# Kernel tuning notes

Hardware: AMD Instinct MI355X
Metric: run time of the kernel (lower is better)

The kernel has to match this reference:

```python
import jax, jax.numpy as jnp
import numpy as np

B, L, D = 2, 2048, 1024
H, QK, V = 8, 128, 128
EPS = 1e-5  # torch GroupNorm default


def setup_inputs() -> dict:
    key = jax.random.key(0)
    ks = jax.random.split(key, 6)
    sequence = jax.random.normal(ks[0], (B, L, D), jnp.float32)
    times = jnp.broadcast_to(jnp.arange(L, dtype=jnp.float32), (B, L))
    shift = D ** -0.5
    scale = 2.0 * shift
    w_q = jax.random.uniform(ks[1], (H, D, QK), jnp.float32) * scale - shift
    w_k = jax.random.uniform(ks[2], (H, D, QK), jnp.float32) * scale - shift
    w_v = jax.random.uniform(ks[3], (H, D, V), jnp.float32) * scale - shift
    out_dims = H * V
    w_g = jax.random.uniform(ks[4], (D, out_dims), jnp.float32) * scale - shift
    shift2 = out_dims ** -0.5
    scale2 = 2.0 * shift2
    w_o = jax.random.uniform(ks[5], (out_dims, out_dims), jnp.float32) * scale2 - shift2
    gn_w = jnp.ones((out_dims,), jnp.float32)
    gn_b = jnp.zeros((out_dims,), jnp.float32)
    return dict(sequence=sequence, times=times, w_q=w_q, w_k=w_k, w_v=w_v,
                w_g=w_g, w_o=w_o, gn_w=gn_w, gn_b=gn_b)


def rotate_by_i(x):
    # pairs (even, odd) -> (-odd, even), interleaved back
    x2 = x.reshape(x.shape[:-1] + (-1, 2))
    real, imag = x2[..., 0], x2[..., 1]
    return jnp.stack([-imag, real], axis=-1).reshape(x.shape)


def reference(sequence, times, w_q, w_k, w_v, w_g, w_o, gn_w, gn_b):
    gammas = 1.0 - 2.0 ** (-5.0 - jnp.arange(H, dtype=jnp.float32))            # (H,)
    thetas = 10000.0 ** (-2.0 * jnp.arange(QK // 2, dtype=jnp.float32) / QK)   # (QK/2,)

    q = jnp.einsum('bld,hdk->hblk', sequence, w_q)  # (H,B,L,QK)
    k = jnp.einsum('bld,hdk->hblk', sequence, w_k)
    v = jnp.einsum('bld,hdv->hblv', sequence, w_v)  # (H,B,L,V)

    # xPos rotor: angles interleaved-duplicated along last dim
    angles = times[..., None] * thetas              # (B,L,QK/2)
    cos = jnp.repeat(jnp.cos(angles), 2, axis=-1)   # (B,L,QK)
    sin = jnp.repeat(jnp.sin(angles), 2, axis=-1)
    q = cos * q + sin * rotate_by_i(q)
    k = cos * k - sin * rotate_by_i(k)

    # causal exponential-decay mask D[n,m] = gamma**(n-m) * (n>=m)
    mat = times[:, :, None] - times[:, None, :]     # (B,L,L)
    mask = mat >= 0
    g4 = gammas[:, None, None, None]                # (H,1,1,1)
    d = jnp.where(mask, g4 ** jnp.where(mask, mat, 0.0), 0.0)  # (H,B,L,L)

    ret = jnp.einsum('hbik,hbjk->hbij', q, k) * d   # (H,B,L,L)
    retention = jnp.einsum('hbij,hbjv->hbiv', ret, v)  # (H,B,L,V)

    # GroupNorm(num_heads, H*V): normalize each head's V channels per token
    r = jnp.transpose(retention, (1, 2, 0, 3))      # (B,L,H,V)
    mean = r.mean(-1, keepdims=True)
    var = r.var(-1, keepdims=True)
    rn = (r - mean) / jnp.sqrt(var + EPS)
    rn = rn * gn_w.reshape(H, V) + gn_b.reshape(H, V)
    rn = rn.reshape(B, L, H * V)

    g = sequence @ w_g
    gate = g * jax.nn.sigmoid(g)                    # swish
    return (gate * rn) @ w_o                        # (B,L,H*V)
```

## Files before the change

### kernel.cpp

```cpp
#include <hip/hip_runtime.h>
#include <stdint.h>

typedef unsigned short u16;
typedef unsigned int   u32;
typedef short  short8 __attribute__((ext_vector_type(8)));
typedef float  f32x4  __attribute__((ext_vector_type(4)));

#define DEV static __device__ __forceinline__

DEV float bf2f(u16 u) { u32 x = ((u32)u) << 16; float f; __builtin_memcpy(&f, &x, 4); return f; }
DEV u16 f2bf(float f) {
  u32 u; __builtin_memcpy(&u, &f, 4);
  return (u16)((u + 0x7FFFu + ((u >> 16) & 1u)) >> 16);
}
DEV bool probe_bf16(const void* times) { return *(const u32*)times == 0x3F800000u; }

DEV void gload16(const u16* g, u16* l) {
  __builtin_amdgcn_global_load_lds(
      (__attribute__((address_space(1))) void*)(u16*)g,
      (__attribute__((address_space(3))) void*)l, 16, 0, 0);
}

DEV f32x4 MFMA(short8 a, short8 b, f32x4 c) {
  return __builtin_amdgcn_mfma_f32_16x16x32_bf16(a, b, c, 0, 0, 0);
}

DEV void gemm128(const u16* Ag, const u16* Bg, int K, u16* sA, u16* sB,
                 f32x4 (&acc)[4][4]) {
  const int tid = threadIdx.x;
  const int lane = tid & 63, w = tid >> 6;
  const int wm = w >> 1, wn = w & 1;
  const int row = lane & 15, quad = lane >> 4;
  f32x4 z = {0.f, 0.f, 0.f, 0.f};
#pragma unroll
  for (int mt = 0; mt < 4; ++mt)
#pragma unroll
    for (int nt = 0; nt < 4; ++nt) acc[mt][nt] = z;

  for (int k0 = 0; k0 < K; k0 += 64) {
    __syncthreads();
#pragma unroll
    for (int i = 0; i < 4; ++i) {
      int c = (w << 2) + i;
      gload16(Ag + (size_t)(c * 8 + (lane >> 3)) * K + k0 + (lane & 7) * 8, sA + c * 544);
      gload16(Bg + (size_t)(c * 8 + (lane >> 3)) * K + k0 + (lane & 7) * 8, sB + c * 544);
    }
    __syncthreads();
#pragma unroll
    for (int kt = 0; kt < 2; ++kt) {
      short8 av[4], bv[4];
#pragma unroll
      for (int t = 0; t < 4; ++t) {
        int m = wm * 64 + t * 16 + row;
        av[t] = *(const short8*)(sA + (m >> 3) * 544 + (m & 7) * 64 + kt * 32 + quad * 8);
        int n = wn * 64 + t * 16 + row;
        bv[t] = *(const short8*)(sB + (n >> 3) * 544 + (n & 7) * 64 + kt * 32 + quad * 8);
      }
#pragma unroll
      for (int mt = 0; mt < 4; ++mt)
#pragma unroll
        for (int nt = 0; nt < 4; ++nt)
          acc[mt][nt] = MFMA(av[mt], bv[nt], acc[mt][nt]);
    }
  }
}

__global__ __launch_bounds__(256) void transpose_kernel(
    const void* wq, const void* wk, const void* wv, const void* wg,
    const void* wo, const void* times, u16* wsT) {
  __shared__ u16 T[128 * 132];
  int s = blockIdx.x, t = blockIdx.y;
  bool isbf = probe_bf16(times);
  const void* src; int ld; size_t off0;
  if (s < 8)       { src = wq; ld = 128;  off0 = (size_t)s * 131072; }
  else if (s < 16) { src = wk; ld = 128;  off0 = (size_t)(s - 8) * 131072; }
  else if (s < 24) { src = wv; ld = 128;  off0 = (size_t)(s - 16) * 131072; }
  else if (s < 32) { src = wg; ld = 1024; off0 = (size_t)(s - 24) * 128; }
  else             { src = wo; ld = 1024; off0 = (size_t)(s - 32) * 128; }
  int d0 = t * 128;
  const u16* s16 = (const u16*)src;
  const float* s32 = (const float*)src;
  for (int pass = 0; pass < 64; ++pass) {
    int idx = pass * 256 + threadIdx.x;
    int dl = idx >> 7, c = idx & 127;
    size_t goff = off0 + (size_t)(d0 + dl) * ld + c;
    T[c * 132 + dl] = isbf ? s16[goff] : f2bf(s32[goff]);
  }
  __syncthreads();
  u16* dst = wsT + (size_t)s * 131072;
  for (int pass = 0; pass < 16; ++pass) {
    int idx = pass * 256 + threadIdx.x;
    int c = idx >> 5, ch = idx & 31;
    uint2 v = *(const uint2*)&T[c * 132 + ch * 4];
    *(uint2*)&dst[(size_t)c * 1024 + d0 + ch * 4] = v;
  }
}

__global__ __launch_bounds__(256) void seq_kernel(const void* seq, const void* times, u16* dst) {
  bool isbf = probe_bf16(times);
  size_t idx = ((size_t)blockIdx.x * 256 + threadIdx.x) * 8;
  if (isbf) {
    *(uint4*)&dst[idx] = *(const uint4*)((const u16*)seq + idx);
  } else {
    const float* s = (const float*)seq;
    u32 a0 = (u32)f2bf(s[idx + 0]) | ((u32)f2bf(s[idx + 1]) << 16);
    u32 a1 = (u32)f2bf(s[idx + 2]) | ((u32)f2bf(s[idx + 3]) << 16);
    u32 a2 = (u32)f2bf(s[idx + 4]) | ((u32)f2bf(s[idx + 5]) << 16);
    u32 a3 = (u32)f2bf(s[idx + 6]) | ((u32)f2bf(s[idx + 7]) << 16);
    uint4 v; v.x = a0; v.y = a1; v.z = a2; v.w = a3;
    *(uint4*)&dst[idx] = v;
  }
}

__global__ __launch_bounds__(256, 2) void proj_kernel(
    const u16* seqb, const void* times, const u16* wsT,
    u16* qws, u16* kws, u16* vtws, u16* gatews) {
  __shared__ __align__(16) u16 smem[17408];
  u16* sA = smem;
  u16* sB = smem + 8704;
  int nb = blockIdx.x, mb = blockIdx.y;
  f32x4 acc[4][4];
  gemm128(seqb + (size_t)mb * 128 * 1024, wsT + (size_t)nb * 131072, 1024, sA, sB, acc);

  const int tid = threadIdx.x, lane = tid & 63, w = tid >> 6;
  const int wm = w >> 1, wn = w & 1, row = lane & 15, quad = lane >> 4;
  const bool isbf = probe_bf16(times);
  const u16* t16 = (const u16*)times;
  const float* t32 = (const float*)times;
  const int b = mb >> 4, l0 = (mb & 15) * 128;

  __syncthreads();

  if (nb < 16) {
    int type = nb >> 3;
    int h = nb & 7;
    float sgnk = type ? -1.f : 1.f;
#pragma unroll
    for (int mt = 0; mt < 4; ++mt) {
#pragma unroll
      for (int nt = 0; nt < 4; ++nt) {
        int c = wn * 64 + nt * 16 + row;
        float theta = exp2f(-0.2076205059304601f * (float)(c >> 1));
        float sgn = (c & 1) ? 1.f : -1.f;
#pragma unroll
        for (int r = 0; r < 4; ++r) {
          int lloc = wm * 64 + mt * 16 + quad * 4 + r;
          float v = acc[mt][nt][r];
          float pv = __shfl_xor(v, 1);
          float tv = isbf ? bf2f(t16[b * 2048 + l0 + lloc]) : t32[b * 2048 + l0 + lloc];
          float rev = theta * tv * 0.15915494309189535f;
          rev -= floorf(rev);
          float sn = __builtin_amdgcn_sinf(rev);
          float cs = __builtin_amdgcn_cosf(rev);
          float ov = cs * v + sgnk * sgn * sn * pv;
          u16 o16 = f2bf(ov);
          int other = __shfl_xor((int)o16, 1);
          if (!(lane & 1))
            *(u32*)&smem[lloc * 136 + c] = (u32)o16 | ((u32)other << 16);
        }
      }
    }
    __syncthreads();
    u16* outp = (type ? kws : qws) + (((size_t)(h * 2 + b) * 2048 + l0) << 7);
#pragma unroll
    for (int p = 0; p < 8; ++p) {
      int idx = p * 256 + tid, rr = idx >> 4, ch = idx & 15;
      *(uint4*)&outp[(size_t)rr * 128 + ch * 8] = *(const uint4*)&smem[rr * 136 + ch * 8];
    }
  } else if (nb < 24) {
    int h = nb & 7;
#pragma unroll
    for (int mt = 0; mt < 4; ++mt) {
      int lb = wm * 64 + mt * 16 + quad * 4;
#pragma unroll
      for (int nt = 0; nt < 4; ++nt) {
        int c = wn * 64 + nt * 16 + row;
        uint2 pk;
        pk.x = (u32)f2bf(acc[mt][nt][0]) | ((u32)f2bf(acc[mt][nt][1]) << 16);
        pk.y = (u32)f2bf(acc[mt][nt][2]) | ((u32)f2bf(acc[mt][nt][3]) << 16);
        *(uint2*)&smem[c * 136 + lb] = pk;
      }
    }
    __syncthreads();
    u16* outp = vtws + (size_t)(h * 2 + b) * 262144 + l0;
#pragma unroll
    for (int p = 0; p < 8; ++p) {
      int idx = p * 256 + tid, cc = idx >> 4, ch = idx & 15;
      *(uint4*)&outp[(size_t)cc * 2048 + ch * 8] = *(const uint4*)&smem[cc * 136 + ch * 8];
    }
  } else {
    int cb = nb - 24;
#pragma unroll
    for (int mt = 0; mt < 4; ++mt) {
#pragma unroll
      for (int nt = 0; nt < 4; ++nt) {
        int c = wn * 64 + nt * 16 + row;
#pragma unroll
        for (int r = 0; r < 4; ++r) {
          int lloc = wm * 64 + mt * 16 + quad * 4 + r;
          float x = acc[mt][nt][r];
          float s = x / (1.f + __expf(-x));
          u16 o16 = f2bf(s);
          int other = __shfl_xor((int)o16, 1);
          if (!(lane & 1))
            *(u32*)&smem[lloc * 136 + c] = (u32)o16 | ((u32)other << 16);
        }
      }
    }
    __syncthreads();
    u16* outp = gatews + (size_t)(mb * 128) * 1024 + (size_t)cb * 128;
#pragma unroll
    for (int p = 0; p < 8; ++p) {
      int idx = p * 256 + tid, rr = idx >> 4, ch = idx & 15;
      *(uint4*)&outp[(size_t)rr * 1024 + ch * 8] = *(const uint4*)&smem[rr * 136 + ch * 8];
    }
  }
}

__global__ __launch_bounds__(256, 2) void retention_kernel(
    const u16* qws, const u16* kws, const u16* vtws, const void* times, float* rws) {
  __shared__ __align__(16) u16 smem[17408 + 16896];
  u16* sKP = smem;
  u16* sV  = smem + 17408;

  const int ib = (int)blockIdx.x >> 1;
  const int par = (int)blockIdx.x & 1;

  const int hb = blockIdx.y;
  const int h = hb >> 1, b = hb & 1;
  const int i0 = ib * 128;
  const int tid = threadIdx.x, lane = tid & 63, w = tid >> 6;
  const int wm = w >> 1, wn = w & 1, row = lane & 15, quad = lane >> 4;
  const bool isbf = probe_bf16(times);
  const u16* t16 = (const u16*)times;
  const float* t32 = (const float*)times;
  const float gamma = 1.f - exp2f(-5.f - (float)h);
  const float l2g = log2f(gamma);

  short8 qf[4][4];
  const u16* qbase = qws + ((size_t)hb * 2048 + i0) * 128;
#pragma unroll
  for (int mt = 0; mt < 4; ++mt)
#pragma unroll
    for (int kt = 0; kt < 4; ++kt)
      qf[mt][kt] = *(const short8*)(qbase + (size_t)(wm * 64 + mt * 16 + row) * 128 + kt * 32 + quad * 8);

  float rpow[4][4];
#pragma unroll
  for (int mt = 0; mt < 4; ++mt)
#pragma unroll
    for (int r = 0; r < 4; ++r) {
      int i = i0 + wm * 64 + mt * 16 + quad * 4 + r;
      float tv = isbf ? bf2f(t16[b * 2048 + i]) : t32[b * 2048 + i];
      rpow[mt][r] = exp2f(l2g * (tv - (float)i0));
    }

  f32x4 z = {0.f, 0.f, 0.f, 0.f};
  f32x4 oacc[4][4];
#pragma unroll
  for (int mt = 0; mt < 4; ++mt)
#pragma unroll
    for (int nt = 0; nt < 4; ++nt) oacc[mt][nt] = z;

  const u16* kbase = kws + (size_t)hb * 262144;
  const u16* vbase = vtws + (size_t)hb * 262144;

  for (int jb = par; jb <= ib; jb += 2) {
    const int j0 = jb * 128;
    if (l2g * (float)(i0 - j0 - 258) < -57.f) continue;
    __syncthreads();
#pragma unroll
    for (int ii = 0; ii < 8; ++ii) {
      int c = w * 8 + ii;
      gload16(kbase + (size_t)(j0 + c * 4 + (lane >> 4)) * 128 + (lane & 15) * 8, sKP + c * 528);
      gload16(vbase + (size_t)(c * 4 + (lane >> 4)) * 2048 + j0 + (lane & 15) * 8, sV + c * 528);
    }
    __syncthreads();

    f32x4 p[4][4];
#pragma unroll
    for (int mt = 0; mt < 4; ++mt)
#pragma unroll
      for (int nt = 0; nt < 4; ++nt) p[mt][nt] = z;
#pragma unroll
    for (int kt = 0; kt < 4; ++kt) {
      short8 bv[4];
#pragma unroll
      for (int nt = 0; nt < 4; ++nt) {
        int jr = wn * 64 + nt * 16 + row;
        bv[nt] = *(const short8*)(sKP + (jr >> 2) * 528 + (jr & 3) * 128 + kt * 32 + quad * 8);
      }
#pragma unroll
      for (int mt = 0; mt < 4; ++mt)
#pragma unroll
        for (int nt = 0; nt < 4; ++nt)
          p[mt][nt] = MFMA(qf[mt][kt], bv[nt], p[mt][nt]);
    }
    __syncthreads();

    float cp[4];
#pragma unroll
    for (int nt = 0; nt < 4; ++nt) {
      int j = j0 + wn * 64 + nt * 16 + row;
      float tv = isbf ? bf2f(t16[b * 2048 + j]) : t32[b * 2048 + j];
      cp[nt] = exp2f(l2g * ((float)i0 - tv));
    }
    bool intra = (jb == ib);
#pragma unroll
    for (int mt = 0; mt < 4; ++mt)
#pragma unroll
      for (int nt = 0; nt < 4; ++nt)
#pragma unroll
        for (int r = 0; r < 4; ++r) {
          float f = rpow[mt][r] * cp[nt];
          float val = p[mt][nt][r] * f;
          if (intra && (f > 1.00001f)) val = 0.f;
          sKP[(wm * 64 + mt * 16 + quad * 4 + r) * 136 + wn * 64 + nt * 16 + row] = f2bf(val);
        }
    __syncthreads();

#pragma unroll
    for (int kt = 0; kt < 4; ++kt) {
      short8 av[4], bv[4];
#pragma unroll
      for (int mt = 0; mt < 4; ++mt)
        av[mt] = *(const short8*)(sKP + (wm * 64 + mt * 16 + row) * 136 + kt * 32 + quad * 8);
#pragma unroll
      for (int nt = 0; nt < 4; ++nt) {
        int v = wn * 64 + nt * 16 + row;
        bv[nt] = *(const short8*)(sV + (v >> 2) * 528 + (v & 3) * 128 + kt * 32 + quad * 8);
      }
#pragma unroll
      for (int mt = 0; mt < 4; ++mt)
#pragma unroll
        for (int nt = 0; nt < 4; ++nt)
          oacc[mt][nt] = MFMA(av[mt], bv[nt], oacc[mt][nt]);
    }
  }

  float* rp = rws + (size_t)par * 4194304 + ((size_t)hb * 2048 + i0) * 128;
#pragma unroll
  for (int mt = 0; mt < 4; ++mt)
#pragma unroll
    for (int nt = 0; nt < 4; ++nt)
#pragma unroll
      for (int r = 0; r < 4; ++r) {
        int i = wm * 64 + mt * 16 + quad * 4 + r;
        int v = wn * 64 + nt * 16 + row;
        rp[(size_t)i * 128 + v] = oacc[mt][nt][r];
      }
}

__global__ __launch_bounds__(256) void norm_kernel(
    const float* rws, const u16* gatews, const void* gnw, const void* gnb,
    const void* times, u16* xws) {
  int tid = threadIdx.x, lane = tid & 63, w = tid >> 6;
  int rid = blockIdx.x * 4 + w;
  int hb = rid >> 11, l = rid & 2047, h = hb >> 1, b = hb & 1;
  bool isbf = probe_bf16(times);
  float2 a0 = *(const float2*)&rws[(size_t)rid * 128 + lane * 2];
  float2 a1 = *(const float2*)&rws[(size_t)4194304 + (size_t)rid * 128 + lane * 2];
  float x0 = a0.x + a1.x, x1 = a0.y + a1.y;
  float s = x0 + x1, ss = x0 * x0 + x1 * x1;
#pragma unroll
  for (int o = 1; o < 64; o <<= 1) { s += __shfl_xor(s, o); ss += __shfl_xor(ss, o); }
  float mean = s * (1.f / 128.f);
  float var = fmaxf(ss * (1.f / 128.f) - mean * mean, 0.f);
  float inv = rsqrtf(var + 1e-5f);
  int c0 = h * 128 + lane * 2;
  float g0, g1, bb0, bb1;
  if (isbf) {
    g0 = bf2f(((const u16*)gnw)[c0]); g1 = bf2f(((const u16*)gnw)[c0 + 1]);
    bb0 = bf2f(((const u16*)gnb)[c0]); bb1 = bf2f(((const u16*)gnb)[c0 + 1]);
  } else {
    g0 = ((const float*)gnw)[c0]; g1 = ((const float*)gnw)[c0 + 1];
    bb0 = ((const float*)gnb)[c0]; bb1 = ((const float*)gnb)[c0 + 1];
  }
  float y0 = (x0 - mean) * inv * g0 + bb0;
  float y1 = (x1 - mean) * inv * g1 + bb1;
  size_t xi = ((size_t)(b * 2048 + l)) * 1024 + c0;
  float gt0 = bf2f(gatews[xi]), gt1 = bf2f(gatews[xi + 1]);
  u32 pk = (u32)f2bf(y0 * gt0) | ((u32)f2bf(y1 * gt1) << 16);
  *(u32*)&xws[xi] = pk;
}

__global__ __launch_bounds__(256, 2) void out_kernel(
    const u16* xws, const u16* wsT, const void* times, void* dout) {
  __shared__ __align__(16) u16 smem[17408];
  u16* sA = smem;
  u16* sB = smem + 8704;
  int nb = blockIdx.x, mb = blockIdx.y;
  f32x4 acc[4][4];
  gemm128(xws + (size_t)mb * 128 * 1024, wsT + (size_t)(32 + nb) * 131072, 1024, sA, sB, acc);
  const int tid = threadIdx.x, lane = tid & 63, w = tid >> 6;
  const int wm = w >> 1, wn = w & 1, row = lane & 15, quad = lane >> 4;
  bool isbf = probe_bf16(times);
  if (isbf) {
    __syncthreads();
#pragma unroll
    for (int mt = 0; mt < 4; ++mt) {
#pragma unroll
      for (int nt = 0; nt < 4; ++nt) {
        int c = wn * 64 + nt * 16 + row;
#pragma unroll
        for (int r = 0; r < 4; ++r) {
          int lloc = wm * 64 + mt * 16 + quad * 4 + r;
          u16 o16 = f2bf(acc[mt][nt][r]);
          int other = __shfl_xor((int)o16, 1);
          if (!(lane & 1))
            *(u32*)&smem[lloc * 136 + c] = (u32)o16 | ((u32)other << 16);
        }
      }
    }
    __syncthreads();
    u16* outp = (u16*)dout + (size_t)(mb * 128) * 1024 + (size_t)nb * 128;
#pragma unroll
    for (int p = 0; p < 8; ++p) {
      int idx = p * 256 + tid, rr = idx >> 4, ch = idx & 15;
      *(uint4*)&outp[(size_t)rr * 1024 + ch * 8] = *(const uint4*)&smem[rr * 136 + ch * 8];
    }
  } else {
#pragma unroll
    for (int mt = 0; mt < 4; ++mt)
#pragma unroll
      for (int nt = 0; nt < 4; ++nt)
#pragma unroll
        for (int r = 0; r < 4; ++r) {
          int i = mb * 128 + wm * 64 + mt * 16 + quad * 4 + r;
          size_t o = (size_t)i * 1024 + nb * 128 + wn * 64 + nt * 16 + row;
          ((float*)dout)[o] = acc[mt][nt][r];
        }
  }
}

extern "C" void kernel_launch(void* const* d_in, const int* in_sizes, int n_in,
                              void* d_out, int out_size, void* d_ws, size_t ws_size,
                              hipStream_t stream) {
  const void* seq   = d_in[0];
  const void* times = d_in[1];
  const void* wq = d_in[2];
  const void* wk = d_in[3];
  const void* wv = d_in[4];
  const void* wg = d_in[5];
  const void* wo = d_in[6];
  const void* gnw = d_in[7];
  const void* gnb = d_in[8];

  u16* ws = (u16*)d_ws;
  u16* wsT    = ws;
  u16* qws    = ws + 5242880;
  u16* kws    = qws + 4194304;
  u16* vtws   = kws + 4194304;
  u16* gatews = vtws + 4194304;
  float* rws  = (float*)(gatews + 4194304);
  u16* seqb   = (u16*)(rws + 8388608);
  u16* xws    = qws;

  transpose_kernel<<<dim3(40, 8), 256, 0, stream>>>(wq, wk, wv, wg, wo, times, wsT);
  seq_kernel<<<dim3(2048), 256, 0, stream>>>(seq, times, seqb);
  proj_kernel<<<dim3(32, 32), 256, 0, stream>>>(seqb, times, wsT, qws, kws, vtws, gatews);
  retention_kernel<<<dim3(32, 16), 256, 0, stream>>>(qws, kws, vtws, times, rws);
  norm_kernel<<<dim3(8192), 256, 0, stream>>>(rws, gatews, gnw, gnb, times, xws);
  out_kernel<<<dim3(8, 32), 256, 0, stream>>>(xws, wsT, times, d_out);
}
```

Baseline: 274.1 us.

## Halve retention query tile to 64 rows and schedule heavy blocks first

The retention kernel now gives each block 64 query rows instead of 128, doubling the grid. Each warp owns 16 rows across all 128 key or value columns, replacing the 2x2 warp split. Block indices are reversed so blocks with the most key tiles launch first, which should improve load balance and CU fill across the causal triangle. The cost is that each K/V tile staged in LDS is reused over half as many query rows, so K/V global traffic and B-fragment LDS reads per MFMA increase.

```diff
diff --git a/kernel.cpp b/kernel.cpp
--- a/kernel.cpp
+++ b/kernel.cpp
@@ -219,53 +219,49 @@
 
 __global__ __launch_bounds__(256, 2) void retention_kernel(
     const u16* qws, const u16* kws, const u16* vtws, const void* times, float* rws) {
-  __shared__ __align__(16) u16 smem[17408 + 16896];
+  __shared__ __align__(16) u16 smem[16896 * 2];
   u16* sKP = smem;
-  u16* sV  = smem + 17408;
-
-  const int ib = (int)blockIdx.x >> 1;
-  const int par = (int)blockIdx.x & 1;
+  u16* sV  = smem + 16896;
+
+  const int x = 63 - (int)blockIdx.x;
+  const int ib = x >> 1;
+  const int par = x & 1;
+  const int jb_max = ib >> 1;
 
   const int hb = blockIdx.y;
   const int h = hb >> 1, b = hb & 1;
-  const int i0 = ib * 128;
+  const int i0 = ib * 64;
   const int tid = threadIdx.x, lane = tid & 63, w = tid >> 6;
-  const int wm = w >> 1, wn = w & 1, row = lane & 15, quad = lane >> 4;
+  const int row = lane & 15, quad = lane >> 4;
   const bool isbf = probe_bf16(times);
   const u16* t16 = (const u16*)times;
   const float* t32 = (const float*)times;
   const float gamma = 1.f - exp2f(-5.f - (float)h);
   const float l2g = log2f(gamma);
 
-  short8 qf[4][4];
-  const u16* qbase = qws + ((size_t)hb * 2048 + i0) * 128;
-#pragma unroll
-  for (int mt = 0; mt < 4; ++mt)
-#pragma unroll
-    for (int kt = 0; kt < 4; ++kt)
-      qf[mt][kt] = *(const short8*)(qbase + (size_t)(wm * 64 + mt * 16 + row) * 128 + kt * 32 + quad * 8);
-
-  float rpow[4][4];
-#pragma unroll
-  for (int mt = 0; mt < 4; ++mt)
-#pragma unroll
-    for (int r = 0; r < 4; ++r) {
-      int i = i0 + wm * 64 + mt * 16 + quad * 4 + r;
-      float tv = isbf ? bf2f(t16[b * 2048 + i]) : t32[b * 2048 + i];
-      rpow[mt][r] = exp2f(l2g * (tv - (float)i0));
-    }
+  short8 qf[4];
+  const u16* qrow = qws + ((size_t)hb * 2048 + i0 + w * 16 + row) * 128;
+#pragma unroll
+  for (int kt = 0; kt < 4; ++kt)
+    qf[kt] = *(const short8*)(qrow + kt * 32 + quad * 8);
+
+  float rpow[4];
+#pragma unroll
+  for (int r = 0; r < 4; ++r) {
+    int i = i0 + w * 16 + quad * 4 + r;
+    float tv = isbf ? bf2f(t16[b * 2048 + i]) : t32[b * 2048 + i];
+    rpow[r] = exp2f(l2g * (tv - (float)i0));
+  }
 
   f32x4 z = {0.f, 0.f, 0.f, 0.f};
-  f32x4 oacc[4][4];
-#pragma unroll
-  for (int mt = 0; mt < 4; ++mt)
-#pragma unroll
-    for (int nt = 0; nt < 4; ++nt) oacc[mt][nt] = z;
+  f32x4 oacc[8];
+#pragma unroll
+  for (int nt = 0; nt < 8; ++nt) oacc[nt] = z;
 
   const u16* kbase = kws + (size_t)hb * 262144;
   const u16* vbase = vtws + (size_t)hb * 262144;
 
-  for (int jb = par; jb <= ib; jb += 2) {
+  for (int jb = par; jb <= jb_max; jb += 2) {
     const int j0 = jb * 128;
     if (l2g * (float)(i0 - j0 - 258) < -57.f) continue;
     __syncthreads();
@@ -277,78 +273,66 @@
     }
     __syncthreads();
 
-    f32x4 p[4][4];
-#pragma unroll
-    for (int mt = 0; mt < 4; ++mt)
-#pragma unroll
-      for (int nt = 0; nt < 4; ++nt) p[mt][nt] = z;
+    f32x4 p[8];
+#pragma unroll
+    for (int nt = 0; nt < 8; ++nt) p[nt] = z;
 #pragma unroll
     for (int kt = 0; kt < 4; ++kt) {
-      short8 bv[4];
-#pragma unroll
-      for (int nt = 0; nt < 4; ++nt) {
-        int jr = wn * 64 + nt * 16 + row;
+      short8 bv[8];
+#pragma unroll
+      for (int nt = 0; nt < 8; ++nt) {
+        int jr = nt * 16 + row;
         bv[nt] = *(const short8*)(sKP + (jr >> 2) * 528 + (jr & 3) * 128 + kt * 32 + quad * 8);
       }
 #pragma unroll
-      for (int mt = 0; mt < 4; ++mt)
-#pragma unroll
-        for (int nt = 0; nt < 4; ++nt)
-          p[mt][nt] = MFMA(qf[mt][kt], bv[nt], p[mt][nt]);
-    }
-    __syncthreads();
-
-    float cp[4];
-#pragma unroll
-    for (int nt = 0; nt < 4; ++nt) {
-      int j = j0 + wn * 64 + nt * 16 + row;
+      for (int nt = 0; nt < 8; ++nt)
+        p[nt] = MFMA(qf[kt], bv[nt], p[nt]);
+    }
+    __syncthreads();
+
+    float cp[8];
+#pragma unroll
+    for (int nt = 0; nt < 8; ++nt) {
+      int j = j0 + nt * 16 + row;
       float tv = isbf ? bf2f(t16[b * 2048 + j]) : t32[b * 2048 + j];
       cp[nt] = exp2f(l2g * ((float)i0 - tv));
     }
-    bool intra = (jb == ib);
-#pragma unroll
-    for (int mt = 0; mt < 4; ++mt)
-#pragma unroll
-      for (int nt = 0; nt < 4; ++nt)
-#pragma unroll
-        for (int r = 0; r < 4; ++r) {
-          float f = rpow[mt][r] * cp[nt];
-          float val = p[mt][nt][r] * f;
-          if (intra && (f > 1.00001f)) val = 0.f;
-          sKP[(wm * 64 + mt * 16 + quad * 4 + r) * 136 + wn * 64 + nt * 16 + row] = f2bf(val);
-        }
+    bool intra = (jb == jb_max);
+#pragma unroll
+    for (int nt = 0; nt < 8; ++nt)
+#pragma unroll
+      for (int r = 0; r < 4; ++r) {
+        float f = rpow[r] * cp[nt];
+        float val = p[nt][r] * f;
+        if (intra && (f > 1.00001f)) val = 0.f;
+        sKP[(w * 16 + quad * 4 + r) * 136 + nt * 16 + row] = f2bf(val);
+      }
     __syncthreads();
 
 #pragma unroll
     for (int kt = 0; kt < 4; ++kt) {
-      short8 av[4], bv[4];
-#pragma unroll
-      for (int mt = 0; mt < 4; ++mt)
-        av[mt] = *(const short8*)(sKP + (wm * 64 + mt * 16 + row) * 136 + kt * 32 + quad * 8);
-#pragma unroll
-      for (int nt = 0; nt < 4; ++nt) {
-        int v = wn * 64 + nt * 16 + row;
+      short8 av = *(const short8*)(sKP + (w * 16 + row) * 136 + kt * 32 + quad * 8);
+      short8 bv[8];
+#pragma unroll
+      for (int nt = 0; nt < 8; ++nt) {
+        int v = nt * 16 + row;
         bv[nt] = *(const short8*)(sV + (v >> 2) * 528 + (v & 3) * 128 + kt * 32 + quad * 8);
       }
 #pragma unroll
-      for (int mt = 0; mt < 4; ++mt)
-#pragma unroll
-        for (int nt = 0; nt < 4; ++nt)
-          oacc[mt][nt] = MFMA(av[mt], bv[nt], oacc[mt][nt]);
+      for (int nt = 0; nt < 8; ++nt)
+        oacc[nt] = MFMA(av, bv[nt], oacc[nt]);
     }
   }
 
   float* rp = rws + (size_t)par * 4194304 + ((size_t)hb * 2048 + i0) * 128;
 #pragma unroll
-  for (int mt = 0; mt < 4; ++mt)
-#pragma unroll
-    for (int nt = 0; nt < 4; ++nt)
-#pragma unroll
-      for (int r = 0; r < 4; ++r) {
-        int i = wm * 64 + mt * 16 + quad * 4 + r;
-        int v = wn * 64 + nt * 16 + row;
-        rp[(size_t)i * 128 + v] = oacc[mt][nt][r];
-      }
+  for (int nt = 0; nt < 8; ++nt)
+#pragma unroll
+    for (int r = 0; r < 4; ++r) {
+      int i = w * 16 + quad * 4 + r;
+      int v = nt * 16 + row;
+      rp[(size_t)i * 128 + v] = oacc[nt][r];
+    }
 }
 
 __global__ __launch_bounds__(256) void norm_kernel(
@@ -459,7 +443,7 @@
   transpose_kernel<<<dim3(40, 8), 256, 0, stream>>>(wq, wk, wv, wg, wo, times, wsT);
   seq_kernel<<<dim3(2048), 256, 0, stream>>>(seq, times, seqb);
   proj_kernel<<<dim3(32, 32), 256, 0, stream>>>(seqb, times, wsT, qws, kws, vtws, gatews);
-  retention_kernel<<<dim3(32, 16), 256, 0, stream>>>(qws, kws, vtws, times, rws);
+  retention_kernel<<<dim3(64, 16), 256, 0, stream>>>(qws, kws, vtws, times, rws);
   norm_kernel<<<dim3(8192), 256, 0, stream>>>(rws, gatews, gnw, gnb, times, xws);
   out_kernel<<<dim3(8, 32), 256, 0, stream>>>(xws, wsT, times, d_out);
 }
```

Result: no change. 278.7 us (+1.7%).

## Halve retention query tile, schedule long blocks first, swizzle K/V LDS chunks

Applied to the files above, without the earlier changes.

The retention kernel now processes 64 query rows per block instead of 128 and doubles the grid, so causal work is spread over more, smaller blocks. Blocks are launched in reverse order so the longest causal rows start first. K and V chunks are rotated per row when written to LDS, and the fragment reads are rotated to match, to reduce LDS bank conflicts. The cost is that K/V tiles are loaded from global memory twice as often per query row, in exchange for better load balance and lower register pressure.

```diff
diff --git a/kernel.cpp b/kernel.cpp
--- a/kernel.cpp
+++ b/kernel.cpp
@@ -219,67 +219,73 @@
 
 __global__ __launch_bounds__(256, 2) void retention_kernel(
     const u16* qws, const u16* kws, const u16* vtws, const void* times, float* rws) {
-  __shared__ __align__(16) u16 smem[17408 + 16896];
+  __shared__ __align__(16) u16 smem[16896 * 2];
   u16* sKP = smem;
-  u16* sV  = smem + 17408;
-
-  const int ib = (int)blockIdx.x >> 1;
-  const int par = (int)blockIdx.x & 1;
+  u16* sV  = smem + 16896;
+
+  const int x = 63 - (int)blockIdx.x;
+  const int ib = x >> 1;
+  const int par = x & 1;
+  const int jb_max = ib >> 1;
 
   const int hb = blockIdx.y;
   const int h = hb >> 1, b = hb & 1;
-  const int i0 = ib * 128;
+  const int i0 = ib * 64;
   const int tid = threadIdx.x, lane = tid & 63, w = tid >> 6;
-  const int wm = w >> 1, wn = w & 1, row = lane & 15, quad = lane >> 4;
+  const int wm = w >> 1, wn = w & 1;
+  const int row = lane & 15, quad = lane >> 4;
   const bool isbf = probe_bf16(times);
   const u16* t16 = (const u16*)times;
   const float* t32 = (const float*)times;
   const float gamma = 1.f - exp2f(-5.f - (float)h);
   const float l2g = log2f(gamma);
 
-  short8 qf[4][4];
-  const u16* qbase = qws + ((size_t)hb * 2048 + i0) * 128;
-#pragma unroll
-  for (int mt = 0; mt < 4; ++mt)
+  short8 qf[2][4];
+  const u16* qbase = qws + ((size_t)hb * 2048 + i0 + wm * 32 + row) * 128;
+#pragma unroll
+  for (int mt = 0; mt < 2; ++mt)
 #pragma unroll
     for (int kt = 0; kt < 4; ++kt)
-      qf[mt][kt] = *(const short8*)(qbase + (size_t)(wm * 64 + mt * 16 + row) * 128 + kt * 32 + quad * 8);
-
-  float rpow[4][4];
-#pragma unroll
-  for (int mt = 0; mt < 4; ++mt)
+      qf[mt][kt] = *(const short8*)(qbase + (size_t)(mt * 16) * 128 + kt * 32 + quad * 8);
+
+  float rpow[2][4];
+#pragma unroll
+  for (int mt = 0; mt < 2; ++mt)
 #pragma unroll
     for (int r = 0; r < 4; ++r) {
-      int i = i0 + wm * 64 + mt * 16 + quad * 4 + r;
+      int i = i0 + wm * 32 + mt * 16 + quad * 4 + r;
       float tv = isbf ? bf2f(t16[b * 2048 + i]) : t32[b * 2048 + i];
       rpow[mt][r] = exp2f(l2g * (tv - (float)i0));
     }
 
   f32x4 z = {0.f, 0.f, 0.f, 0.f};
-  f32x4 oacc[4][4];
-#pragma unroll
-  for (int mt = 0; mt < 4; ++mt)
+  f32x4 oacc[2][4];
+#pragma unroll
+  for (int mt = 0; mt < 2; ++mt)
 #pragma unroll
     for (int nt = 0; nt < 4; ++nt) oacc[mt][nt] = z;
 
   const u16* kbase = kws + (size_t)hb * 262144;
   const u16* vbase = vtws + (size_t)hb * 262144;
 
-  for (int jb = par; jb <= ib; jb += 2) {
+  const int srho = lane >> 4;
+  const int schunk = ((lane & 15) - srho) & 15;
+
+  for (int jb = par; jb <= jb_max; jb += 2) {
     const int j0 = jb * 128;
     if (l2g * (float)(i0 - j0 - 258) < -57.f) continue;
     __syncthreads();
 #pragma unroll
     for (int ii = 0; ii < 8; ++ii) {
       int c = w * 8 + ii;
-      gload16(kbase + (size_t)(j0 + c * 4 + (lane >> 4)) * 128 + (lane & 15) * 8, sKP + c * 528);
-      gload16(vbase + (size_t)(c * 4 + (lane >> 4)) * 2048 + j0 + (lane & 15) * 8, sV + c * 528);
-    }
-    __syncthreads();
-
-    f32x4 p[4][4];
-#pragma unroll
-    for (int mt = 0; mt < 4; ++mt)
+      gload16(kbase + (size_t)(j0 + c * 4 + srho) * 128 + schunk * 8, sKP + c * 528);
+      gload16(vbase + (size_t)(c * 4 + srho) * 2048 + j0 + schunk * 8, sV + c * 528);
+    }
+    __syncthreads();
+
+    f32x4 p[2][4];
+#pragma unroll
+    for (int mt = 0; mt < 2; ++mt)
 #pragma unroll
       for (int nt = 0; nt < 4; ++nt) p[mt][nt] = z;
 #pragma unroll
@@ -288,10 +294,11 @@
 #pragma unroll
       for (int nt = 0; nt < 4; ++nt) {
         int jr = wn * 64 + nt * 16 + row;
-        bv[nt] = *(const short8*)(sKP + (jr >> 2) * 528 + (jr & 3) * 128 + kt * 32 + quad * 8);
-      }
-#pragma unroll
-      for (int mt = 0; mt < 4; ++mt)
+        bv[nt] = *(const short8*)(sKP + (jr >> 2) * 528 + (jr & 3) * 128 +
+                                  (((kt * 4 + quad) + (jr & 3)) & 15) * 8);
+      }
+#pragma unroll
+      for (int mt = 0; mt < 2; ++mt)
 #pragma unroll
         for (int nt = 0; nt < 4; ++nt)
           p[mt][nt] = MFMA(qf[mt][kt], bv[nt], p[mt][nt]);
@@ -305,9 +312,9 @@
       float tv = isbf ? bf2f(t16[b * 2048 + j]) : t32[b * 2048 + j];
       cp[nt] = exp2f(l2g * ((float)i0 - tv));
     }
-    bool intra = (jb == ib);
-#pragma unroll
-    for (int mt = 0; mt < 4; ++mt)
+    bool intra = (jb == jb_max);
+#pragma unroll
+    for (int mt = 0; mt < 2; ++mt)
 #pragma unroll
       for (int nt = 0; nt < 4; ++nt)
 #pragma unroll
@@ -315,23 +322,24 @@
           float f = rpow[mt][r] * cp[nt];
           float val = p[mt][nt][r] * f;
           if (intra && (f > 1.00001f)) val = 0.f;
-          sKP[(wm * 64 + mt * 16 + quad * 4 + r) * 136 + wn * 64 + nt * 16 + row] = f2bf(val);
+          sKP[(wm * 32 + mt * 16 + quad * 4 + r) * 136 + wn * 64 + nt * 16 + row] = f2bf(val);
         }
     __syncthreads();
 
 #pragma unroll
     for (int kt = 0; kt < 4; ++kt) {
-      short8 av[4], bv[4];
-#pragma unroll
-      for (int mt = 0; mt < 4; ++mt)
-        av[mt] = *(const short8*)(sKP + (wm * 64 + mt * 16 + row) * 136 + kt * 32 + quad * 8);
-#pragma unroll
-      for (int nt = 0; nt < 4; ++nt) {
-        int v = wn * 64 + nt * 16 + row;
-        bv[nt] = *(const short8*)(sV + (v >> 2) * 528 + (v & 3) * 128 + kt * 32 + quad * 8);
-      }
-#pragma unroll
-      for (int mt = 0; mt < 4; ++mt)
+      short8 av[2], bv[4];
+#pragma unroll
+      for (int mt = 0; mt < 2; ++mt)
+        av[mt] = *(const short8*)(sKP + (wm * 32 + mt * 16 + row) * 136 + kt * 32 + quad * 8);
+#pragma unroll
+      for (int nt = 0; nt < 4; ++nt) {
+        int vv = wn * 64 + nt * 16 + row;
+        bv[nt] = *(const short8*)(sV + (vv >> 2) * 528 + (vv & 3) * 128 +
+                                  (((kt * 4 + quad) + (vv & 3)) & 15) * 8);
+      }
+#pragma unroll
+      for (int mt = 0; mt < 2; ++mt)
 #pragma unroll
         for (int nt = 0; nt < 4; ++nt)
           oacc[mt][nt] = MFMA(av[mt], bv[nt], oacc[mt][nt]);
@@ -340,12 +348,12 @@
 
   float* rp = rws + (size_t)par * 4194304 + ((size_t)hb * 2048 + i0) * 128;
 #pragma unroll
-  for (int mt = 0; mt < 4; ++mt)
+  for (int mt = 0; mt < 2; ++mt)
 #pragma unroll
     for (int nt = 0; nt < 4; ++nt)
 #pragma unroll
       for (int r = 0; r < 4; ++r) {
-        int i = wm * 64 + mt * 16 + quad * 4 + r;
+        int i = wm * 32 + mt * 16 + quad * 4 + r;
         int v = wn * 64 + nt * 16 + row;
         rp[(size_t)i * 128 + v] = oacc[mt][nt][r];
       }
@@ -459,7 +467,7 @@
   transpose_kernel<<<dim3(40, 8), 256, 0, stream>>>(wq, wk, wv, wg, wo, times, wsT);
   seq_kernel<<<dim3(2048), 256, 0, stream>>>(seq, times, seqb);
   proj_kernel<<<dim3(32, 32), 256, 0, stream>>>(seqb, times, wsT, qws, kws, vtws, gatews);
-  retention_kernel<<<dim3(32, 16), 256, 0, stream>>>(qws, kws, vtws, times, rws);
+  retention_kernel<<<dim3(64, 16), 256, 0, stream>>>(qws, kws, vtws, times, rws);
   norm_kernel<<<dim3(8192), 256, 0, stream>>>(rws, gatews, gnw, gnb, times, xws);
   out_kernel<<<dim3(8, 32), 256, 0, stream>>>(xws, wsT, times, d_out);
 }
```

Result: faster. 258.7 us (-5.6%).
